# Kernel optimization log

Hardware: AMD Instinct MI355X
Metric: run time of the kernel (lower is better)

Reference implementation:

```python
import jax, jax.numpy as jnp
import numpy as np

B, S, T, E, H = 2, 2048, 2048, 1024, 16
HD = E // H  # head_dim = 64


def setup_inputs() -> dict:
    key = jax.random.key(0)
    ks = jax.random.split(key, 12)
    sc = 1.0 / np.sqrt(E)
    inp = {
        "query": jax.random.normal(ks[0], (B, S, E), jnp.float32),
        "key": jax.random.normal(ks[1], (B, T, E), jnp.float32),
        "value": jax.random.normal(ks[2], (B, T, E), jnp.float32),
        "attn_mask": jnp.ones((S, T), jnp.int32),
        # nn.Linear params: y = x @ W.T + b
        "Wq": jax.random.normal(ks[3], (E, E), jnp.float32) * sc,
        "bq": jax.random.normal(ks[4], (E,), jnp.float32) * sc,
        "Wk": jax.random.normal(ks[5], (E, E), jnp.float32) * sc,
        "bk": jax.random.normal(ks[6], (E,), jnp.float32) * sc,
        "Wv": jax.random.normal(ks[7], (E, E), jnp.float32) * sc,
        "bv": jax.random.normal(ks[8], (E,), jnp.float32) * sc,
        "Wo": jax.random.normal(ks[9], (E, E), jnp.float32) * sc,
        "bo": jax.random.normal(ks[10], (E,), jnp.float32) * sc,
    }
    return inp


def reference(query, key, value, attn_mask, Wq, bq, Wk, bk, Wv, bv, Wo, bo):
    N, Sq, Ed = query.shape
    Tk = key.shape[1]
    # projections (torch Linear: x @ W.T + b)
    q = query @ Wq.T + bq
    k = key @ Wk.T + bk
    v = value @ Wv.T + bv
    # split heads -> (N, H, S, HD)
    q = q.reshape(N, Sq, H, HD).transpose(0, 2, 1, 3)
    k = k.reshape(N, Tk, H, HD).transpose(0, 2, 1, 3)
    v = v.reshape(N, Tk, H, HD).transpose(0, 2, 1, 3)
    # scaled dot-product scores: (N, H, S, T)
    energy = jnp.einsum("nhsd,nhtd->nhst", q, k) / jnp.sqrt(jnp.float32(HD))
    energy = jnp.where(attn_mask[None, None, :, :] == 0, -jnp.inf, energy)
    attn = jax.nn.softmax(energy, axis=3)
    # dropout is identity in eval mode
    out = jnp.einsum("nhst,nhtd->nshd", attn, v).reshape(N, Sq, Ed)
    return out @ Wo.T + bo
```

## Files before the change

### kernel.cpp

```cpp
#include <hip/hip_runtime.h>

typedef __attribute__((ext_vector_type(8))) short short8;
typedef __attribute__((ext_vector_type(4))) float f32x4;
typedef __attribute__((ext_vector_type(16))) float f32x16;

#define DEV __device__ __forceinline__

constexpr int Bb = 2, Ss = 2048, Tt = 2048, Ee = 1024, Hh = 16, HDd = 64;
constexpr int Mm = Bb * Ss;
constexpr size_t NX = (size_t)Mm * Ee;
constexpr size_t NW = (size_t)Ee * Ee;

constexpr size_t OFF_XQ   = 0;
constexpr size_t OFF_XK   = OFF_XQ + NX * 2;
constexpr size_t OFF_XV   = OFF_XK + NX * 2;
constexpr size_t OFF_WQ   = OFF_XV + NX * 2;
constexpr size_t OFF_WK   = OFF_WQ + NW * 2;
constexpr size_t OFF_WV   = OFF_WK + NW * 2;
constexpr size_t OFF_WO   = OFF_WV + NW * 2;
constexpr size_t OFF_QH   = OFF_WO + NW * 2;
constexpr size_t OFF_KH   = OFF_QH + NX * 2;
constexpr size_t OFF_VH   = OFF_KH + NX * 2;
constexpr size_t OFF_OB   = OFF_VH + NX * 2;
constexpr size_t OFF_FLAG = OFF_OB + NX * 2;

DEV unsigned short f2bf(float f) {
  union { float f; unsigned u; } v; v.f = f;
  unsigned r = v.u + 0x7fffu + ((v.u >> 16) & 1u);
  return (unsigned short)(r >> 16);
}

#define GLDS16(g, l) __builtin_amdgcn_global_load_lds(                         \
    (const __attribute__((address_space(1))) void*)(g),                        \
    (__attribute__((address_space(3))) void*)(l), 16, 0, 0)

#define PLSWAP(a, b) asm("v_permlane32_swap_b32 %0, %1" : "+v"(a), "+v"(b))
#define CVTPK(d, lo, hi_) asm("v_cvt_pk_bf16_f32 %0, %1, %2" : "=v"(d) : "v"(lo), "v"(hi_))

#if __has_builtin(__builtin_amdgcn_exp2f)
#define EXP2(x) __builtin_amdgcn_exp2f(x)
#else
#define EXP2(x) __expf((x) * 0.69314718f)
#endif

constexpr float SCLQ = 0.18033688f;

__global__ __launch_bounds__(256) void prep_kernel(
    const float* __restrict__ q, const float* __restrict__ k, const float* __restrict__ v,
    const float* __restrict__ wq, const float* __restrict__ wk,
    const float* __restrict__ wv, const float* __restrict__ wo,
    const int* __restrict__ mask,
    unsigned short* __restrict__ Xq, unsigned short* __restrict__ Xk, unsigned short* __restrict__ Xv,
    unsigned short* __restrict__ Wqb, unsigned short* __restrict__ Wkb,
    unsigned short* __restrict__ Wvb, unsigned short* __restrict__ Wob,
    int* __restrict__ flagZero)
{
  constexpr size_t NXv = NX / 4, NWv = NW / 4;
  constexpr size_t tot = 4 * NXv + 4 * NWv;
  for (size_t u = (size_t)blockIdx.x * blockDim.x + threadIdx.x; u < tot;
       u += (size_t)gridDim.x * blockDim.x) {
    if (u < 3 * NXv) {
      const float* src; unsigned short* dst; size_t off;
      if (u < NXv)            { src = q; dst = Xq; off = u; }
      else if (u < 2 * NXv)   { src = k; dst = Xk; off = u - NXv; }
      else                    { src = v; dst = Xv; off = u - 2 * NXv; }
      float4 f = ((const float4*)src)[off];
      ushort4 o; o.x = f2bf(f.x); o.y = f2bf(f.y); o.z = f2bf(f.z); o.w = f2bf(f.w);
      ((ushort4*)dst)[off] = o;
    } else if (u < 3 * NXv + 4 * NWv) {
      size_t uu = u - 3 * NXv;
      int wsel = (int)(uu / NWv); size_t off = uu % NWv;
      const float* src = wsel == 0 ? wq : wsel == 1 ? wk : wsel == 2 ? wv : wo;
      unsigned short* dst = wsel == 0 ? Wqb : wsel == 1 ? Wkb : wsel == 2 ? Wvb : Wob;
      float4 f = ((const float4*)src)[off];
      ushort4 o; o.x = f2bf(f.x); o.y = f2bf(f.y); o.z = f2bf(f.z); o.w = f2bf(f.w);
      ((ushort4*)dst)[off] = o;
    } else {
      size_t off = u - 3 * NXv - 4 * NWv;
      int4 m = ((const int4*)mask)[off];
      if (m.x == 0 || m.y == 0 || m.z == 0 || m.w == 0) *flagZero = 1;
    }
  }
}

DEV void gemm128(const unsigned short* __restrict__ A, const unsigned short* __restrict__ Bm,
                 unsigned short (*Asm)[128 * 32], unsigned short (*Bsm)[128 * 32],
                 f32x4 acc[4][4], int K)
{
  const int t = threadIdx.x;
  const int w = t >> 6, lane = t & 63;
  const int l15 = lane & 15, l4 = lane >> 4;
  const int wm = w >> 1, wn = w & 1;
  const int srow = lane >> 2;
  const int skc  = (lane & 3) * 8;
#pragma unroll
  for (int mi = 0; mi < 4; ++mi)
#pragma unroll
    for (int ni = 0; ni < 4; ++ni) acc[mi][ni] = (f32x4){0.f, 0.f, 0.f, 0.f};

#define GSTAGE(d, k0)                                                              \
  {                                                                                \
    GLDS16(A  + (size_t)(w * 16 + srow) * K + (k0) + skc,      Asm[d] + w * 512);  \
    GLDS16(A  + (size_t)(64 + w * 16 + srow) * K + (k0) + skc, Asm[d] + 2048 + w * 512); \
    GLDS16(Bm + (size_t)(w * 16 + srow) * K + (k0) + skc,      Bsm[d] + w * 512);  \
    GLDS16(Bm + (size_t)(64 + w * 16 + srow) * K + (k0) + skc, Bsm[d] + 2048 + w * 512); \
  }

  GSTAGE(0, 0)
  int it = 0;
  for (int k0 = 0; k0 < K; k0 += 32, ++it) {
    const int cur = it & 1;
    asm volatile("s_waitcnt vmcnt(0)" ::: "memory");
    __builtin_amdgcn_s_barrier();
    if (k0 + 32 < K) GSTAGE(cur ^ 1, k0 + 32)

    short8 af[4], bf[4];
#pragma unroll
    for (int mi = 0; mi < 4; ++mi)
      af[mi] = *(const short8*)&Asm[cur][(wm * 64 + mi * 16 + l15) * 32 + l4 * 8];
#pragma unroll
    for (int ni = 0; ni < 4; ++ni)
      bf[ni] = *(const short8*)&Bsm[cur][(wn * 64 + ni * 16 + l15) * 32 + l4 * 8];
    __builtin_amdgcn_s_setprio(1);
#pragma unroll
    for (int mi = 0; mi < 4; ++mi)
#pragma unroll
      for (int ni = 0; ni < 4; ++ni)
        acc[mi][ni] = __builtin_amdgcn_mfma_f32_16x16x32_bf16(af[mi], bf[ni], acc[mi][ni], 0, 0, 0);
    __builtin_amdgcn_s_setprio(0);
  }
#undef GSTAGE
}

__global__ __launch_bounds__(256, 4) void gemm_qkv(
    const unsigned short* __restrict__ Xq, const unsigned short* __restrict__ Xk,
    const unsigned short* __restrict__ Xv,
    const unsigned short* __restrict__ Wqb, const unsigned short* __restrict__ Wkb,
    const unsigned short* __restrict__ Wvb,
    const float* __restrict__ bq, const float* __restrict__ bk, const float* __restrict__ bv,
    unsigned short* __restrict__ Qh, unsigned short* __restrict__ Kh, unsigned short* __restrict__ Vh)
{
  __shared__ unsigned short Asm[2][128 * 32], Bsm[2][128 * 32];
  const int z = blockIdx.z;
  const unsigned short* A  = (z == 0) ? Xq  : (z == 1) ? Xk  : Xv;
  const unsigned short* Bw = (z == 0) ? Wqb : (z == 1) ? Wkb : Wvb;
  const float* bias        = (z == 0) ? bq  : (z == 1) ? bk  : bv;
  unsigned short* Out      = (z == 0) ? Qh  : (z == 1) ? Kh  : Vh;
  const int by = blockIdx.y, bx = blockIdx.x;
  f32x4 acc[4][4];
  gemm128(A + (size_t)by * 128 * Ee, Bw + (size_t)bx * 128 * Ee, Asm, Bsm, acc, Ee);
  const int t = threadIdx.x, w = t >> 6, lane = t & 63, l15 = lane & 15, l4 = lane >> 4;
  const int wm = w >> 1, wn = w & 1;
  if (z < 2) {
    const float osc = (z == 0) ? SCLQ : 1.0f;
#pragma unroll
    for (int ni = 0; ni < 4; ++ni) {
      int col = bx * 128 + wn * 64 + ni * 16 + l15;
      float bcol = bias[col];
      int h = col >> 6, hd = col & 63;
#pragma unroll
      for (int mi = 0; mi < 4; ++mi) {
#pragma unroll
        for (int r = 0; r < 4; ++r) {
          int row = by * 128 + wm * 64 + mi * 16 + l4 * 4 + r;
          int b = row >> 11, s = row & 2047;
          Out[(((size_t)(b * Hh + h)) * Ss + s) * HDd + hd] = f2bf((acc[mi][ni][r] + bcol) * osc);
        }
      }
    }
  } else {
#pragma unroll
    for (int ni = 0; ni < 4; ++ni) {
      int col = bx * 128 + wn * 64 + ni * 16 + l15;
      float bcol = bias[col];
      int h = col >> 6, hd = col & 63;
#pragma unroll
      for (int mi = 0; mi < 4; ++mi) {
        int row = by * 128 + wm * 64 + mi * 16 + l4 * 4;
        int b = row >> 11, s = row & 2047;
        ushort4 pk;
        pk.x = f2bf(acc[mi][ni][0] + bcol); pk.y = f2bf(acc[mi][ni][1] + bcol);
        pk.z = f2bf(acc[mi][ni][2] + bcol); pk.w = f2bf(acc[mi][ni][3] + bcol);
        *(ushort4*)&Out[((size_t)((b * Hh + h) * HDd + hd)) * Ss + s] = pk;
      }
    }
  }
}

__global__ __launch_bounds__(256, 4) void gemm_out(
    const unsigned short* __restrict__ Ob, const unsigned short* __restrict__ Wob,
    const float* __restrict__ bo, float* __restrict__ out)
{
  __shared__ unsigned short Asm[2][128 * 32], Bsm[2][128 * 32];
  const int by = blockIdx.y, bx = blockIdx.x;
  f32x4 acc[4][4];
  gemm128(Ob + (size_t)by * 128 * Ee, Wob + (size_t)bx * 128 * Ee, Asm, Bsm, acc, Ee);
  const int t = threadIdx.x, w = t >> 6, lane = t & 63, l15 = lane & 15, l4 = lane >> 4;
  const int wm = w >> 1, wn = w & 1;
#pragma unroll
  for (int ni = 0; ni < 4; ++ni) {
    int col = bx * 128 + wn * 64 + ni * 16 + l15;
    float bcol = bo[col];
#pragma unroll
    for (int mi = 0; mi < 4; ++mi) {
#pragma unroll
      for (int r = 0; r < 4; ++r) {
        int row = by * 128 + wm * 64 + mi * 16 + l4 * 4 + r;
        out[(size_t)row * Ee + col] = acc[mi][ni][r] + bcol;
      }
    }
  }
}

__global__ __launch_bounds__(256) void attn_kernel(
    const unsigned short* __restrict__ Qh, const unsigned short* __restrict__ Kh,
    const unsigned short* __restrict__ Vh, const int* __restrict__ mask,
    const int* __restrict__ flagZero, unsigned short* __restrict__ Ob)
{
  __shared__ unsigned short Ks[2][128 * 64];
  __shared__ unsigned short Vs[2][64 * 128];
  const int bh = blockIdx.y, qt = blockIdx.x;
  const int tid = threadIdx.x, w = tid >> 6, lane = tid & 63;
  const int l31 = lane & 31, hi = lane >> 5;
  const bool useMask = (*flagZero != 0);
  const size_t bhBase = (size_t)bh * Ss * HDd;
  const int s0 = qt * 128 + w * 32;

  short8 qf[4];
#pragma unroll
  for (int ks = 0; ks < 4; ++ks)
    qf[ks] = *(const short8*)&Qh[bhBase + (size_t)(s0 + l31) * 64 + ks * 16 + hi * 8];

  f32x16 o0, o1, Z16;
#pragma unroll
  for (int r = 0; r < 16; ++r) { o0[r] = 0.f; o1[r] = 0.f; Z16[r] = 0.f; }
  float l_r = 0.f;

  const int kRow = tid >> 3, kG = (tid & 7) ^ (kRow & 7);
  const int vRow = tid >> 4, vG = (tid & 15) ^ (vRow & 15);

#define STAGE(d, kt2)                                                                         \
  {                                                                                           \
    _Pragma("unroll")                                                                         \
    for (int i = 0; i < 4; ++i)                                                               \
      GLDS16(Kh + bhBase + (size_t)((kt2) + i * 32 + kRow) * 64 + kG * 8,                     \
             &Ks[d][0] + (i * 256 + w * 64) * 8);                                             \
    _Pragma("unroll")                                                                         \
    for (int i = 0; i < 4; ++i)                                                               \
      GLDS16(Vh + bhBase + (size_t)(i * 16 + vRow) * Ss + (kt2) + vG * 8,                     \
             &Vs[d][0] + (i * 256 + w * 64) * 8);                                             \
  }

  STAGE(0, 0)

  for (int t = 0; t < 16; ++t) {
    const int kt2 = t * 128, cur = t & 1;
    asm volatile("s_waitcnt vmcnt(0)" ::: "memory");
    __builtin_amdgcn_s_barrier();
    if (t + 1 < 16) STAGE(cur ^ 1, kt2 + 128)

    const unsigned short* Kc = &Ks[cur][0];
    const unsigned short* Vc = &Vs[cur][0];

    f32x16 p[4];
    __builtin_amdgcn_s_setprio(1);
#pragma unroll
    for (int g4 = 0; g4 < 4; ++g4) {
      const int row = g4 * 32 + l31;
      short8 ka = *(const short8*)&Kc[row * 64 + ((hi ^ (l31 & 7)) * 8)];
      p[g4] = __builtin_amdgcn_mfma_f32_32x32x16_bf16(ka, qf[0], Z16, 0, 0, 0);
#pragma unroll
      for (int ks = 1; ks < 4; ++ks) {
        short8 kb = *(const short8*)&Kc[row * 64 + (((ks * 2 + hi) ^ (l31 & 7)) * 8)];
        p[g4] = __builtin_amdgcn_mfma_f32_32x32x16_bf16(kb, qf[ks], p[g4], 0, 0, 0);
      }
    }
    __builtin_amdgcn_s_setprio(0);

    if (useMask) {
      int sg = s0 + l31;
#pragma unroll
      for (int g4 = 0; g4 < 4; ++g4)
#pragma unroll
        for (int r = 0; r < 16; ++r) {
          int tg = kt2 + g4 * 32 + (r & 3) + 8 * (r >> 2) + 4 * hi;
          if (mask[(size_t)sg * Tt + tg] == 0) p[g4][r] = -1e30f;
        }
    }

#pragma unroll
    for (int g4 = 0; g4 < 4; ++g4)
#pragma unroll
      for (int r = 0; r < 16; ++r) p[g4][r] = EXP2(p[g4][r]);

    float psg[4];
#pragma unroll
    for (int g4 = 0; g4 < 4; ++g4) {
      float a0 = (p[g4][0] + p[g4][1]) + (p[g4][2] + p[g4][3]);
      float a1 = (p[g4][4] + p[g4][5]) + (p[g4][6] + p[g4][7]);
      float a2 = (p[g4][8] + p[g4][9]) + (p[g4][10] + p[g4][11]);
      float a3 = (p[g4][12] + p[g4][13]) + (p[g4][14] + p[g4][15]);
      psg[g4] = (a0 + a1) + (a2 + a3);
    }
    l_r += (psg[0] + psg[1]) + (psg[2] + psg[3]);

    short8 pa[8];
#pragma unroll
    for (int g4 = 0; g4 < 4; ++g4)
#pragma unroll
      for (int h2 = 0; h2 < 2; ++h2) {
        unsigned a0, a1, b0, b1; const int bse = h2 * 8;
        CVTPK(a0, p[g4][bse + 0], p[g4][bse + 1]);
        CVTPK(a1, p[g4][bse + 2], p[g4][bse + 3]);
        CVTPK(b0, p[g4][bse + 4], p[g4][bse + 5]);
        CVTPK(b1, p[g4][bse + 6], p[g4][bse + 7]);
        PLSWAP(a0, b0); PLSWAP(a1, b1);
        union { unsigned u[4]; short8 s; } cc;
        cc.u[0] = a0; cc.u[1] = a1; cc.u[2] = b0; cc.u[3] = b1;
        pa[g4 * 2 + h2] = cc.s;
      }

    __builtin_amdgcn_s_setprio(1);
#pragma unroll
    for (int kb = 0; kb < 8; ++kb) {
      const int sl = ((kb * 2 + hi) ^ (l31 & 15)) * 8;
      short8 vf0 = *(const short8*)&Vc[l31 * 128 + sl];
      short8 vf1 = *(const short8*)&Vc[(32 + l31) * 128 + sl];
      o0 = __builtin_amdgcn_mfma_f32_32x32x16_bf16(pa[kb], vf0, o0, 0, 0, 0);
      o1 = __builtin_amdgcn_mfma_f32_32x32x16_bf16(pa[kb], vf1, o1, 0, 0, 0);
    }
    __builtin_amdgcn_s_setprio(0);
  }
#undef STAGE

  float lt = l_r + __shfl_xor(l_r, 32);
  float linv = lt > 0.f ? 1.0f / lt : 0.f;
  const int b = bh >> 4, h = bh & 15;
#pragma unroll
  for (int r = 0; r < 16; ++r) {
    int sr = (r & 3) + 8 * (r >> 2) + 4 * hi;
    float li = __shfl(linv, sr);
    size_t rowbase = (size_t)(b * Ss + s0 + sr) * Ee + h * 64;
    Ob[rowbase + l31]      = f2bf(o0[r] * li);
    Ob[rowbase + 32 + l31] = f2bf(o1[r] * li);
  }
}

extern "C" void kernel_launch(void* const* d_in, const int* in_sizes, int n_in,
                              void* d_out, int out_size, void* d_ws, size_t ws_size,
                              hipStream_t stream) {
  const float* q   = (const float*)d_in[0];
  const float* k   = (const float*)d_in[1];
  const float* v   = (const float*)d_in[2];
  const int*  msk  = (const int*)d_in[3];
  const float* Wq  = (const float*)d_in[4];
  const float* bq  = (const float*)d_in[5];
  const float* Wk  = (const float*)d_in[6];
  const float* bk  = (const float*)d_in[7];
  const float* Wv  = (const float*)d_in[8];
  const float* bv  = (const float*)d_in[9];
  const float* Wo  = (const float*)d_in[10];
  const float* bo  = (const float*)d_in[11];
  float* out = (float*)d_out;

  char* ws = (char*)d_ws;
  unsigned short* Xq  = (unsigned short*)(ws + OFF_XQ);
  unsigned short* Xk  = (unsigned short*)(ws + OFF_XK);
  unsigned short* Xv  = (unsigned short*)(ws + OFF_XV);
  unsigned short* Wqb = (unsigned short*)(ws + OFF_WQ);
  unsigned short* Wkb = (unsigned short*)(ws + OFF_WK);
  unsigned short* Wvb = (unsigned short*)(ws + OFF_WV);
  unsigned short* Wob = (unsigned short*)(ws + OFF_WO);
  unsigned short* Qh  = (unsigned short*)(ws + OFF_QH);
  unsigned short* Kh  = (unsigned short*)(ws + OFF_KH);
  unsigned short* Vh  = (unsigned short*)(ws + OFF_VH);
  unsigned short* Ob  = (unsigned short*)(ws + OFF_OB);
  int* flagZero       = (int*)(ws + OFF_FLAG);

  hipMemsetAsync(flagZero, 0, 4, stream);
  prep_kernel<<<4096, 256, 0, stream>>>(q, k, v, Wq, Wk, Wv, Wo, msk,
                                        Xq, Xk, Xv, Wqb, Wkb, Wvb, Wob, flagZero);
  gemm_qkv<<<dim3(8, 32, 3), 256, 0, stream>>>(Xq, Xk, Xv, Wqb, Wkb, Wvb,
                                               bq, bk, bv, Qh, Kh, Vh);
  attn_kernel<<<dim3(16, 32), 256, 0, stream>>>(Qh, Kh, Vh, msk, flagZero, Ob);
  gemm_out<<<dim3(8, 32), 256, 0, stream>>>(Ob, Wob, bo, out);
}
```

Measured before the change: 136.7 us.

## Split attention key range across wave pairs and widen output GEMM to 512 threads

```diff
diff --git a/kernel.cpp b/kernel.cpp
--- a/kernel.cpp
+++ b/kernel.cpp
@@ -187,44 +187,84 @@
   }
 }
 
-__global__ __launch_bounds__(256, 4) void gemm_out(
+__global__ __launch_bounds__(512) void gemm_out(
     const unsigned short* __restrict__ Ob, const unsigned short* __restrict__ Wob,
     const float* __restrict__ bo, float* __restrict__ out)
 {
   __shared__ unsigned short Asm[2][128 * 32], Bsm[2][128 * 32];
+  const int tid = threadIdx.x, w = tid >> 6, lane = tid & 63;
+  const int l15 = lane & 15, l4 = lane >> 4;
+  const int wm = w >> 1, wn = w & 1;
   const int by = blockIdx.y, bx = blockIdx.x;
-  f32x4 acc[4][4];
-  gemm128(Ob + (size_t)by * 128 * Ee, Wob + (size_t)bx * 128 * Ee, Asm, Bsm, acc, Ee);
-  const int t = threadIdx.x, w = t >> 6, lane = t & 63, l15 = lane & 15, l4 = lane >> 4;
-  const int wm = w >> 1, wn = w & 1;
+  const unsigned short* A  = Ob  + (size_t)by * 128 * Ee;
+  const unsigned short* Bm = Wob + (size_t)bx * 128 * Ee;
+  const int grow = tid >> 2, gk = (tid & 3) * 8;
+  f32x4 acc[2][4];
+#pragma unroll
+  for (int mi = 0; mi < 2; ++mi)
+#pragma unroll
+    for (int ni = 0; ni < 4; ++ni) acc[mi][ni] = (f32x4){0.f, 0.f, 0.f, 0.f};
+
+#define GSTAGE2(d, k0)                                                   \
+  {                                                                      \
+    GLDS16(A  + (size_t)grow * Ee + (k0) + gk, Asm[d] + w * 512);        \
+    GLDS16(Bm + (size_t)grow * Ee + (k0) + gk, Bsm[d] + w * 512);        \
+  }
+
+  GSTAGE2(0, 0)
+  int it = 0;
+  for (int k0 = 0; k0 < Ee; k0 += 32, ++it) {
+    const int cur = it & 1;
+    asm volatile("s_waitcnt vmcnt(0)" ::: "memory");
+    __builtin_amdgcn_s_barrier();
+    if (k0 + 32 < Ee) GSTAGE2(cur ^ 1, k0 + 32)
+
+    short8 af[2], bf[4];
+#pragma unroll
+    for (int mi = 0; mi < 2; ++mi)
+      af[mi] = *(const short8*)&Asm[cur][(wm * 32 + mi * 16 + l15) * 32 + l4 * 8];
+#pragma unroll
+    for (int ni = 0; ni < 4; ++ni)
+      bf[ni] = *(const short8*)&Bsm[cur][(wn * 64 + ni * 16 + l15) * 32 + l4 * 8];
+    __builtin_amdgcn_s_setprio(1);
+#pragma unroll
+    for (int mi = 0; mi < 2; ++mi)
+#pragma unroll
+      for (int ni = 0; ni < 4; ++ni)
+        acc[mi][ni] = __builtin_amdgcn_mfma_f32_16x16x32_bf16(af[mi], bf[ni], acc[mi][ni], 0, 0, 0);
+    __builtin_amdgcn_s_setprio(0);
+  }
+#undef GSTAGE2
+
 #pragma unroll
   for (int ni = 0; ni < 4; ++ni) {
     int col = bx * 128 + wn * 64 + ni * 16 + l15;
     float bcol = bo[col];
 #pragma unroll
-    for (int mi = 0; mi < 4; ++mi) {
+    for (int mi = 0; mi < 2; ++mi) {
 #pragma unroll
       for (int r = 0; r < 4; ++r) {
-        int row = by * 128 + wm * 64 + mi * 16 + l4 * 4 + r;
+        int row = by * 128 + wm * 32 + mi * 16 + l4 * 4 + r;
         out[(size_t)row * Ee + col] = acc[mi][ni][r] + bcol;
       }
     }
   }
 }
 
-__global__ __launch_bounds__(256) void attn_kernel(
+__global__ __launch_bounds__(256, 4) void attn_kernel(
     const unsigned short* __restrict__ Qh, const unsigned short* __restrict__ Kh,
     const unsigned short* __restrict__ Vh, const int* __restrict__ mask,
     const int* __restrict__ flagZero, unsigned short* __restrict__ Ob)
 {
-  __shared__ unsigned short Ks[2][128 * 64];
-  __shared__ unsigned short Vs[2][64 * 128];
+  __shared__ unsigned short Ks[2][64 * 64];
+  __shared__ unsigned short Vs[2][64 * 64];
   const int bh = blockIdx.y, qt = blockIdx.x;
   const int tid = threadIdx.x, w = tid >> 6, lane = tid & 63;
   const int l31 = lane & 31, hi = lane >> 5;
+  const int g = w >> 1, p = w & 1;
   const bool useMask = (*flagZero != 0);
   const size_t bhBase = (size_t)bh * Ss * HDd;
-  const int s0 = qt * 128 + w * 32;
+  const int s0 = qt * 64 + g * 32;
 
   short8 qf[4];
 #pragma unroll
@@ -236,43 +276,41 @@
   for (int r = 0; r < 16; ++r) { o0[r] = 0.f; o1[r] = 0.f; Z16[r] = 0.f; }
   float l_r = 0.f;
 
-  const int kRow = tid >> 3, kG = (tid & 7) ^ (kRow & 7);
-  const int vRow = tid >> 4, vG = (tid & 15) ^ (vRow & 15);
+  const int cRow = tid >> 3, cG = (tid & 7) ^ (cRow & 7);
 
 #define STAGE(d, kt2)                                                                         \
   {                                                                                           \
     _Pragma("unroll")                                                                         \
-    for (int i = 0; i < 4; ++i)                                                               \
-      GLDS16(Kh + bhBase + (size_t)((kt2) + i * 32 + kRow) * 64 + kG * 8,                     \
+    for (int i = 0; i < 2; ++i)                                                               \
+      GLDS16(Kh + bhBase + (size_t)((kt2) + i * 32 + cRow) * 64 + cG * 8,                     \
              &Ks[d][0] + (i * 256 + w * 64) * 8);                                             \
     _Pragma("unroll")                                                                         \
-    for (int i = 0; i < 4; ++i)                                                               \
-      GLDS16(Vh + bhBase + (size_t)(i * 16 + vRow) * Ss + (kt2) + vG * 8,                     \
+    for (int i = 0; i < 2; ++i)                                                               \
+      GLDS16(Vh + bhBase + (size_t)(i * 32 + cRow) * Ss + (kt2) + cG * 8,                     \
              &Vs[d][0] + (i * 256 + w * 64) * 8);                                             \
   }
 
   STAGE(0, 0)
 
-  for (int t = 0; t < 16; ++t) {
-    const int kt2 = t * 128, cur = t & 1;
+  for (int t = 0; t < 32; ++t) {
+    const int kt2 = t * 64, cur = t & 1;
     asm volatile("s_waitcnt vmcnt(0)" ::: "memory");
     __builtin_amdgcn_s_barrier();
-    if (t + 1 < 16) STAGE(cur ^ 1, kt2 + 128)
+    if (t + 1 < 32) STAGE(cur ^ 1, kt2 + 64)
 
     const unsigned short* Kc = &Ks[cur][0];
     const unsigned short* Vc = &Vs[cur][0];
-
-    f32x16 p[4];
+    const int trow = p * 32 + l31;
+
+    f32x16 pr;
     __builtin_amdgcn_s_setprio(1);
-#pragma unroll
-    for (int g4 = 0; g4 < 4; ++g4) {
-      const int row = g4 * 32 + l31;
-      short8 ka = *(const short8*)&Kc[row * 64 + ((hi ^ (l31 & 7)) * 8)];
-      p[g4] = __builtin_amdgcn_mfma_f32_32x32x16_bf16(ka, qf[0], Z16, 0, 0, 0);
+    {
+      short8 ka = *(const short8*)&Kc[trow * 64 + ((hi ^ (l31 & 7)) * 8)];
+      pr = __builtin_amdgcn_mfma_f32_32x32x16_bf16(ka, qf[0], Z16, 0, 0, 0);
 #pragma unroll
       for (int ks = 1; ks < 4; ++ks) {
-        short8 kb = *(const short8*)&Kc[row * 64 + (((ks * 2 + hi) ^ (l31 & 7)) * 8)];
-        p[g4] = __builtin_amdgcn_mfma_f32_32x32x16_bf16(kb, qf[ks], p[g4], 0, 0, 0);
+        short8 kb = *(const short8*)&Kc[trow * 64 + (((ks * 2 + hi) ^ (l31 & 7)) * 8)];
+        pr = __builtin_amdgcn_mfma_f32_32x32x16_bf16(kb, qf[ks], pr, 0, 0, 0);
       }
     }
     __builtin_amdgcn_s_setprio(0);
@@ -280,52 +318,40 @@
     if (useMask) {
       int sg = s0 + l31;
 #pragma unroll
-      for (int g4 = 0; g4 < 4; ++g4)
-#pragma unroll
-        for (int r = 0; r < 16; ++r) {
-          int tg = kt2 + g4 * 32 + (r & 3) + 8 * (r >> 2) + 4 * hi;
-          if (mask[(size_t)sg * Tt + tg] == 0) p[g4][r] = -1e30f;
-        }
-    }
-
-#pragma unroll
-    for (int g4 = 0; g4 < 4; ++g4)
-#pragma unroll
-      for (int r = 0; r < 16; ++r) p[g4][r] = EXP2(p[g4][r]);
-
-    float psg[4];
-#pragma unroll
-    for (int g4 = 0; g4 < 4; ++g4) {
-      float a0 = (p[g4][0] + p[g4][1]) + (p[g4][2] + p[g4][3]);
-      float a1 = (p[g4][4] + p[g4][5]) + (p[g4][6] + p[g4][7]);
-      float a2 = (p[g4][8] + p[g4][9]) + (p[g4][10] + p[g4][11]);
-      float a3 = (p[g4][12] + p[g4][13]) + (p[g4][14] + p[g4][15]);
-      psg[g4] = (a0 + a1) + (a2 + a3);
-    }
-    l_r += (psg[0] + psg[1]) + (psg[2] + psg[3]);
-
-    short8 pa[8];
-#pragma unroll
-    for (int g4 = 0; g4 < 4; ++g4)
-#pragma unroll
-      for (int h2 = 0; h2 < 2; ++h2) {
-        unsigned a0, a1, b0, b1; const int bse = h2 * 8;
-        CVTPK(a0, p[g4][bse + 0], p[g4][bse + 1]);
-        CVTPK(a1, p[g4][bse + 2], p[g4][bse + 3]);
-        CVTPK(b0, p[g4][bse + 4], p[g4][bse + 5]);
-        CVTPK(b1, p[g4][bse + 6], p[g4][bse + 7]);
-        PLSWAP(a0, b0); PLSWAP(a1, b1);
-        union { unsigned u[4]; short8 s; } cc;
-        cc.u[0] = a0; cc.u[1] = a1; cc.u[2] = b0; cc.u[3] = b1;
-        pa[g4 * 2 + h2] = cc.s;
+      for (int r = 0; r < 16; ++r) {
+        int tg = kt2 + p * 32 + (r & 3) + 8 * (r >> 2) + 4 * hi;
+        if (mask[(size_t)sg * Tt + tg] == 0) pr[r] = -1e30f;
       }
+    }
+
+#pragma unroll
+    for (int r = 0; r < 16; ++r) pr[r] = EXP2(pr[r]);
+    float a0 = (pr[0] + pr[1]) + (pr[2] + pr[3]);
+    float a1 = (pr[4] + pr[5]) + (pr[6] + pr[7]);
+    float a2 = (pr[8] + pr[9]) + (pr[10] + pr[11]);
+    float a3 = (pr[12] + pr[13]) + (pr[14] + pr[15]);
+    l_r += (a0 + a1) + (a2 + a3);
+
+    short8 pa[2];
+#pragma unroll
+    for (int h2 = 0; h2 < 2; ++h2) {
+      unsigned c0, c1, d0, d1; const int bse = h2 * 8;
+      CVTPK(c0, pr[bse + 0], pr[bse + 1]);
+      CVTPK(c1, pr[bse + 2], pr[bse + 3]);
+      CVTPK(d0, pr[bse + 4], pr[bse + 5]);
+      CVTPK(d1, pr[bse + 6], pr[bse + 7]);
+      PLSWAP(c0, d0); PLSWAP(c1, d1);
+      union { unsigned u[4]; short8 s; } cc;
+      cc.u[0] = c0; cc.u[1] = c1; cc.u[2] = d0; cc.u[3] = d1;
+      pa[h2] = cc.s;
+    }
 
     __builtin_amdgcn_s_setprio(1);
 #pragma unroll
-    for (int kb = 0; kb < 8; ++kb) {
-      const int sl = ((kb * 2 + hi) ^ (l31 & 15)) * 8;
-      short8 vf0 = *(const short8*)&Vc[l31 * 128 + sl];
-      short8 vf1 = *(const short8*)&Vc[(32 + l31) * 128 + sl];
+    for (int kb = 0; kb < 2; ++kb) {
+      const int sl0 = ((p * 4 + kb * 2 + hi) ^ (l31 & 7)) * 8;
+      short8 vf0 = *(const short8*)&Vc[l31 * 64 + sl0];
+      short8 vf1 = *(const short8*)&Vc[(32 + l31) * 64 + sl0];
       o0 = __builtin_amdgcn_mfma_f32_32x32x16_bf16(pa[kb], vf0, o0, 0, 0, 0);
       o1 = __builtin_amdgcn_mfma_f32_32x32x16_bf16(pa[kb], vf1, o1, 0, 0, 0);
     }
@@ -333,16 +359,33 @@
   }
 #undef STAGE
 
+  __syncthreads();
+
+  float* Ox = (float*)&Ks[0][0];
+  float* Ml = (float*)&Vs[0][0];
   float lt = l_r + __shfl_xor(l_r, 32);
-  float linv = lt > 0.f ? 1.0f / lt : 0.f;
-  const int b = bh >> 4, h = bh & 15;
-#pragma unroll
-  for (int r = 0; r < 16; ++r) {
-    int sr = (r & 3) + 8 * (r >> 2) + 4 * hi;
-    float li = __shfl(linv, sr);
-    size_t rowbase = (size_t)(b * Ss + s0 + sr) * Ee + h * 64;
-    Ob[rowbase + l31]      = f2bf(o0[r] * li);
-    Ob[rowbase + 32 + l31] = f2bf(o1[r] * li);
+  if (p == 1) {
+#pragma unroll
+    for (int r = 0; r < 16; ++r) {
+      int sr = (r & 3) + 8 * (r >> 2) + 4 * hi;
+      Ox[g * 2048 + sr * 64 + l31]      = o0[r];
+      Ox[g * 2048 + sr * 64 + 32 + l31] = o1[r];
+    }
+    if (hi == 0) Ml[g * 32 + l31] = lt;
+  }
+  __syncthreads();
+  if (p == 0) {
+    const int b = bh >> 4, h = bh & 15;
+    float ltot = lt + Ml[g * 32 + l31];
+    float linv = ltot > 0.f ? 1.0f / ltot : 0.f;
+#pragma unroll
+    for (int r = 0; r < 16; ++r) {
+      int sr = (r & 3) + 8 * (r >> 2) + 4 * hi;
+      float li = __shfl(linv, sr);
+      size_t rowbase = (size_t)(b * Ss + s0 + sr) * Ee + h * 64;
+      Ob[rowbase + l31]      = f2bf((o0[r] + Ox[g * 2048 + sr * 64 + l31]) * li);
+      Ob[rowbase + 32 + l31] = f2bf((o1[r] + Ox[g * 2048 + sr * 64 + 32 + l31]) * li);
+    }
   }
 }
 
@@ -382,6 +425,6 @@
                                         Xq, Xk, Xv, Wqb, Wkb, Wvb, Wob, flagZero);
   gemm_qkv<<<dim3(8, 32, 3), 256, 0, stream>>>(Xq, Xk, Xv, Wqb, Wkb, Wvb,
                                                bq, bk, bv, Qh, Kh, Vh);
-  attn_kernel<<<dim3(16, 32), 256, 0, stream>>>(Qh, Kh, Vh, msk, flagZero, Ob);
-  gemm_out<<<dim3(8, 32), 256, 0, stream>>>(Ob, Wob, bo, out);
-}
+  attn_kernel<<<dim3(32, 32), 256, 0, stream>>>(Qh, Kh, Vh, msk, flagZero, Ob);
+  gemm_out<<<dim3(8, 32), 512, 0, stream>>>(Ob, Wob, bo, out);
+}
```

Measured after the change: 135.0 us. No clear change (-1.3%).
